# Kernel optimization log

Hardware: AMD Instinct MI355X
Metric: run time of the kernel (lower is better)

## Reference

```python
import math
import jax
import jax.numpy as jnp
import numpy as np

MUL = 32            # multiplicity of 0e and 1o in irreps_in/out
N_NODES = 50000
N_EDGES = 800000
N_BASIS = 10
N_HID = 100
NUM_NEIGHBORS = 16.0


def setup_inputs() -> dict:
    key = jax.random.key(0)
    ks = jax.random.split(key, 14)
    return {
        "node_input": jax.random.normal(ks[0], (N_NODES, 4 * MUL), jnp.float32),
        "node_attr": jnp.ones((N_NODES, 1), jnp.float32),
        "edge_src": jax.random.randint(ks[1], (N_EDGES,), 0, N_NODES, dtype=jnp.int32),
        "edge_dst": jax.random.randint(ks[2], (N_EDGES,), 0, N_NODES, dtype=jnp.int32),
        "edge_attr": jax.random.normal(ks[3], (N_EDGES, 4), jnp.float32),
        "edge_length_embedded": jax.random.uniform(ks[4], (N_EDGES, N_BASIS), dtype=jnp.float32),
        "W_sc0": jax.random.normal(ks[5], (MUL, MUL), jnp.float32),
        "W_sc1": jax.random.normal(ks[6], (MUL, MUL), jnp.float32),
        "W_l10": jax.random.normal(ks[7], (MUL, MUL), jnp.float32),
        "W_l11": jax.random.normal(ks[8], (MUL, MUL), jnp.float32),
        "W_l20": jax.random.normal(ks[9], (2 * MUL, MUL), jnp.float32),
        "W_l21": jax.random.normal(ks[10], (2 * MUL, MUL), jnp.float32),
        "W_fc1": jax.random.normal(ks[11], (N_BASIS, N_HID), jnp.float32),
        "W_fc2": jax.random.normal(ks[12], (N_HID, 4 * MUL), jnp.float32),
    }


def _fctp(x0, x1, attr, W0, W1):
    """FullyConnectedTensorProduct with a 1x0e attr: per-irrep linear * scalar attr.
    x0: [N,U], x1: [N,U,3], attr: [N,1]. Path norm alpha = 1/sqrt(fan_in)."""
    inv = 1.0 / math.sqrt(W0.shape[0])
    o0 = attr * (x0 @ W0) * inv                                    # [N,W]
    o1 = attr[:, :, None] * jnp.einsum("nud,uw->nwd", x1, W1) * inv  # [N,W,3]
    return o0, o1


def _forward(node_input, node_attr, edge_attr, edge_length_embedded,
             W_sc0, W_sc1, W_l10, W_l11, W_l20, W_l21, W_fc1, W_fc2,
             edge_src, edge_dst):
    N = node_input.shape[0]
    x0 = node_input[:, :MUL]                       # [N,32]  0e
    x1 = node_input[:, MUL:].reshape(N, MUL, 3)    # [N,32,3] 1o

    # self-connection and lin1 (both attr is scalar 0e)
    s0, s1 = _fctp(x0, x1, node_attr, W_sc0, W_sc1)
    y0, y1 = _fctp(x0, x1, node_attr, W_l10, W_l11)

    # radial MLP -> per-edge uvu weights (weight_numel = 4*MUL)
    h = jax.nn.silu(edge_length_embedded @ W_fc1 * (1.0 / math.sqrt(N_BASIS)))
    w = h @ W_fc2 * (1.0 / math.sqrt(N_HID))       # [E,128]
    w1, w2, w3, w4 = (w[:, 0*MUL:1*MUL], w[:, 1*MUL:2*MUL],
                      w[:, 2*MUL:3*MUL], w[:, 3*MUL:4*MUL])

    # gather source node features per edge
    x0s = y0[edge_src]                              # [E,32]
    x1s = y1[edge_src]                              # [E,32,3]
    ea0 = edge_attr[:, :1]                          # [E,1]   0e
    ea1 = edge_attr[:, 1:]                          # [E,3]   1o

    # segmented uvu tensor product (CG for lmax=1, component norm)
    mid0a = w1 * x0s * ea0                                         # 0e x 0e -> 0e
    mid0b = w4 * jnp.einsum("eum,em->eu", x1s, ea1) * (1.0 / math.sqrt(3.0))  # 1o x 1o -> 0e
    mid1a = (w2 * x0s)[:, :, None] * ea1[:, None, :]               # 0e x 1o -> 1o
    mid1b = w3[:, :, None] * x1s * ea0[:, None, :]                 # 1o x 0e -> 1o
    E = edge_attr.shape[0]
    edge_features = jnp.concatenate(
        [mid0a, mid0b, mid1a.reshape(E, -1), mid1b.reshape(E, -1)], axis=1)  # [E,256]

    # scatter-add to destination nodes
    agg = jax.ops.segment_sum(edge_features, edge_dst, num_segments=N)
    agg = agg * (1.0 / math.sqrt(NUM_NEIGHBORS))

    m0 = agg[:, :2 * MUL]                           # [N,64]  0e part of irreps_mid
    m1 = agg[:, 2 * MUL:].reshape(N, 2 * MUL, 3)    # [N,64,3] 1o part
    z0, z1 = _fctp(m0, m1, node_attr, W_l20, W_l21)

    # sc output_mask is all ones (every output irrep reachable)
    c_s = math.sin(math.pi / 8.0)
    c_x = math.cos(math.pi / 8.0)
    out0 = c_s * s0 + c_x * z0
    out1 = c_s * s1 + c_x * z1
    return jnp.concatenate([out0, out1.reshape(N, -1)], axis=1)   # [N,128]


def reference(node_input, node_attr, edge_src, edge_dst, edge_attr, edge_length_embedded,
              W_sc0, W_sc1, W_l10, W_l11, W_l20, W_l21, W_fc1, W_fc2):
    return _forward(node_input, node_attr, edge_attr, edge_length_embedded,
                    W_sc0, W_sc1, W_l10, W_l11, W_l20, W_l21, W_fc1, W_fc2,
                    edge_src, edge_dst)
```

## Files before the change

### kernel.cpp

```cpp
#include <hip/hip_runtime.h>
#include <hip/hip_bf16.h>

#define MUL 32
#define F4 128
#define NB 10
#define NH 100
#define EROW 136
#define FROW 72
#define XROW 136
#define REC 48

#define INV_SQRT32 0.17677669529663687f
#define INV_SQRT10 0.31622776601683794f
#define INV_SQRT100 0.1f
#define INV_SQRT3 0.5773502691896258f
#define AGG_SCALE 0.25f
#define INV8 0.125f
#define C_S 0.3826834323650898f
#define C_X 0.9238795325112867f
#define CS32 (C_S * INV_SQRT32)
#define CX8 (C_X * INV8)

typedef __attribute__((ext_vector_type(8))) short short8;
typedef __attribute__((ext_vector_type(4))) float float4v;

__device__ __forceinline__ float bf2f(__hip_bfloat16 v) { return __bfloat162float(v); }
__device__ __forceinline__ unsigned short f2b(float x) {
    __hip_bfloat16 b = __float2bfloat16(x);
    return *(unsigned short*)&b;
}
__device__ __forceinline__ float b2f(unsigned short u) {
    __hip_bfloat16 b;
    *(unsigned short*)&b = u;
    return __bfloat162float(b);
}
__device__ __forceinline__ float ldin(const void* p, size_t i, int f) {
    return f ? ((const float*)p)[i] : bf2f(((const __hip_bfloat16*)p)[i]);
}

__device__ __forceinline__ void barrier_lds() {
    asm volatile("s_waitcnt lgkmcnt(0)" ::: "memory");
    __builtin_amdgcn_s_barrier();
}

__global__ void detect_dtype_kernel(const void* __restrict__ node_attr, int* __restrict__ flag) {
    unsigned w = *(const unsigned*)node_attr;
    *flag = (w == 0x3F800000u) ? 1 : 0;
}

__global__ __launch_bounds__(256) void prep_kernel(
    const void* __restrict__ Wfc1,
    const void* __restrict__ Wfc2,
    const void* __restrict__ Wl20,
    const void* __restrict__ Wl21,
    const void* __restrict__ Wl10,
    const void* __restrict__ Wl11,
    const void* __restrict__ Wsc0,
    const void* __restrict__ Wsc1,
    const int* __restrict__ flagp,
    unsigned short* __restrict__ w1t,
    unsigned short* __restrict__ w2t,
    unsigned short* __restrict__ w20t,
    unsigned short* __restrict__ w21t,
    unsigned short* __restrict__ w10t,
    unsigned short* __restrict__ w11t,
    unsigned short* __restrict__ wsc0t,
    unsigned short* __restrict__ wsc1t)
{
    int f = *flagp;
    int gi = blockIdx.x * 256 + threadIdx.x;
    if (gi < 128 * 128) {
        int n = gi >> 7, k = gi & 127;
        w2t[gi] = (k < NH) ? f2b(ldin(Wfc2, (size_t)k * 128 + n, f)) : 0;
    }
    if (gi < 32 * 64) {
        int v = gi >> 6, u = gi & 63;
        w20t[gi] = f2b(ldin(Wl20, (size_t)u * 32 + v, f));
        w21t[gi] = f2b(ldin(Wl21, (size_t)u * 32 + v, f));
    }
    if (gi < 112 * 32) {
        int n = gi >> 5, k = gi & 31;
        w1t[gi] = (k < NB && n < NH) ? f2b(ldin(Wfc1, (size_t)k * NH + n, f)) : 0;
    }
    if (gi < 1024) {
        int c = gi >> 5, u = gi & 31;
        w10t[gi]  = f2b(ldin(Wl10, (size_t)u * 32 + c, f));
        w11t[gi]  = f2b(ldin(Wl11, (size_t)u * 32 + c, f));
        wsc0t[gi] = f2b(ldin(Wsc0, (size_t)u * 32 + c, f));
        wsc1t[gi] = f2b(ldin(Wsc1, (size_t)u * 32 + c, f));
    }
}

__global__ __launch_bounds__(256) void hist_kernel(
    const int* __restrict__ edst, int* __restrict__ cnt, int E)
{
    int i = blockIdx.x * 256 + threadIdx.x;
    if (i < E) atomicAdd(&cnt[edst[i]], 1);
}

__global__ __launch_bounds__(1024) void scanA_kernel(
    int* __restrict__ cnt, int* __restrict__ bsum, int N)
{
    __shared__ int wsum[16];
    int t = threadIdx.x, lane = t & 63, wid = t >> 6;
    int i = blockIdx.x * 1024 + t;
    int v = (i < N) ? cnt[i] : 0;
    int x = v;
#pragma unroll
    for (int d = 1; d < 64; d <<= 1) { int yv = __shfl_up(x, d); if (lane >= d) x += yv; }
    if (lane == 63) wsum[wid] = x;
    __syncthreads();
    if (wid == 0 && lane < 16) {
        int s = wsum[lane];
#pragma unroll
        for (int d = 1; d < 16; d <<= 1) { int yv = __shfl_up(s, d); if (lane >= d) s += yv; }
        wsum[lane] = s;
    }
    __syncthreads();
    int pre = (wid > 0 ? wsum[wid - 1] : 0);
    if (i < N) cnt[i] = pre + x - v;
    if (t == 0) bsum[blockIdx.x] = wsum[15];
}

__global__ __launch_bounds__(64) void scanB_kernel(int* __restrict__ bsum, int nb)
{
    int t = threadIdx.x;
    int carry = 0;
    for (int c0 = 0; c0 < nb; c0 += 64) {
        int idx = c0 + t;
        int v = (idx < nb) ? bsum[idx] : 0;
        int x = v;
#pragma unroll
        for (int d = 1; d < 64; d <<= 1) { int yv = __shfl_up(x, d); if (t >= d) x += yv; }
        if (idx < nb) bsum[idx] = carry + x - v;
        carry += __shfl(x, 63);
    }
}

__global__ __launch_bounds__(1024) void scanC_kernel(
    int* __restrict__ cnt, const int* __restrict__ bsum, int N)
{
    int i = blockIdx.x * 1024 + threadIdx.x;
    if (i < N) cnt[i] += bsum[blockIdx.x];
}

__global__ __launch_bounds__(256) void scatter_build_kernel(
    const int* __restrict__ edst,
    const int* __restrict__ esrc,
    const void* __restrict__ eattr,
    const void* __restrict__ ele,
    const int* __restrict__ flagp,
    int* __restrict__ cnt,
    unsigned char* __restrict__ rec, int E)
{
    int i = blockIdx.x * 256 + threadIdx.x;
    if (i >= E) return;
    int f = *flagp;
    int d = edst[i];
    int p = atomicAdd(&cnt[d], 1);

    unsigned e0 = f2b(ldin(ele, (size_t)i * NB + 0, f));
    unsigned e1 = f2b(ldin(ele, (size_t)i * NB + 1, f));
    unsigned e2 = f2b(ldin(ele, (size_t)i * NB + 2, f));
    unsigned e3 = f2b(ldin(ele, (size_t)i * NB + 3, f));
    unsigned e4 = f2b(ldin(ele, (size_t)i * NB + 4, f));
    unsigned e5 = f2b(ldin(ele, (size_t)i * NB + 5, f));
    unsigned e6 = f2b(ldin(ele, (size_t)i * NB + 6, f));
    unsigned e7 = f2b(ldin(ele, (size_t)i * NB + 7, f));
    unsigned e8 = f2b(ldin(ele, (size_t)i * NB + 8, f));
    unsigned e9 = f2b(ldin(ele, (size_t)i * NB + 9, f));
    float ea0 = ldin(eattr, (size_t)i * 4 + 0, f);
    float ea1 = ldin(eattr, (size_t)i * 4 + 1, f);
    float ea2 = ldin(eattr, (size_t)i * 4 + 2, f);
    float ea3 = ldin(eattr, (size_t)i * 4 + 3, f);

    unsigned char* r = rec + (size_t)p * REC;
    *(int4*)(r + 0)  = make_int4(esrc[i], d, (int)(e0 | (e1 << 16)), (int)(e2 | (e3 << 16)));
    *(int4*)(r + 16) = make_int4((int)(e4 | (e5 << 16)), (int)(e6 | (e7 << 16)), (int)(e8 | (e9 << 16)), 0);
    *(float4*)(r + 32) = make_float4(ea0, ea1, ea2, ea3);
}

__global__ __launch_bounds__(256) void node_y_kernel(
    const void* __restrict__ node_input,
    const void* __restrict__ node_attr,
    const unsigned short* __restrict__ w10t,
    const unsigned short* __restrict__ w11t,
    const int* __restrict__ flagp,
    unsigned short* __restrict__ y, int N)
{
    __shared__ __align__(16) unsigned short sXp[64 * XROW];
    __shared__ float sAt[64];
    int f = *flagp;
    int t = threadIdx.x;
    int n0 = blockIdx.x * 64;
    for (int i = t; i < 64 * 128; i += 256) {
        int n = i >> 7, c = i & 127;
        float v = (n0 + n < N) ? ldin(node_input, (size_t)(n0 + n) * F4 + c, f) : 0.f;
        int slot = (c < 32) ? c : 32 + ((c - 32) % 3) * 32 + (c - 32) / 3;
        sXp[n * XROW + slot] = f2b(v);
    }
    if (t < 64) sAt[t] = (n0 + t < N) ? ldin(node_attr, n0 + t, f) : 0.f;
    __syncthreads();

    int w = t >> 6, lane = t & 63, lm = lane & 15, quad = lane >> 4;
    int arow = (w * 16 + lm) * XROW;
    short8 ax0 = *(const short8*)(sXp + arow + quad * 8);
    short8 ax1[3];
#pragma unroll
    for (int d = 0; d < 3; d++)
        ax1[d] = *(const short8*)(sXp + arow + 32 + d * 32 + quad * 8);

#pragma unroll
    for (int seg = 0; seg < 4; seg++) {
        short8 a = (seg == 0) ? ax0 : ax1[seg - 1];
        const unsigned short* wt = (seg == 0) ? w10t : w11t;
#pragma unroll
        for (int nt = 0; nt < 2; nt++) {
            float4v c1 = (float4v){0.f, 0.f, 0.f, 0.f};
            short8 b = *(const short8*)(wt + (nt * 16 + lm) * 32 + quad * 8);
            c1 = __builtin_amdgcn_mfma_f32_16x16x32_bf16(a, b, c1, 0, 0, 0);
#pragma unroll
            for (int r = 0; r < 4; r++) {
                int nl = w * 16 + quad * 4 + r;
                int n = n0 + nl;
                if (n < N)
                    y[(size_t)n * F4 + seg * 32 + nt * 16 + lm] =
                        f2b(c1[r] * sAt[nl] * INV_SQRT32);
            }
        }
    }
}

#define SM_ELEB  0
#define SM_HW    4096
#define SM_DST   21504
#define SM_TOTAL 21760

__global__ __launch_bounds__(256, 6) void fused_edge_kernel(
    const unsigned char* __restrict__ rec,
    const unsigned short* __restrict__ y,
    const unsigned short* __restrict__ w1t,
    const unsigned short* __restrict__ w2t,
    const unsigned short* __restrict__ w20t,
    const unsigned short* __restrict__ w21t,
    float* __restrict__ agg,
    int E)
{
    __shared__ __align__(16) char smem[SM_TOTAL];
    unsigned short* sEleB = (unsigned short*)(smem + SM_ELEB);
    unsigned short* sHW = (unsigned short*)(smem + SM_HW);
    int* sDst = (int*)(smem + SM_DST);

    int t = threadIdx.x;
    int base = blockIdx.x * 64;
    int ne = E - base;
    if (ne > 64) ne = 64;

    int w = t >> 6, lane = t & 63;
    int lm = lane & 15, quad = lane >> 4;
    int em = w * 16 + lm;

    int src = (em < ne) ? *(const int*)(rec + (size_t)(base + em) * REC) : 0;
    float4 ea4 = (em < ne) ? *(const float4*)(rec + (size_t)(base + em) * REC + 32)
                           : make_float4(0.f, 0.f, 0.f, 0.f);
    const unsigned short* yrg = y + (size_t)src * 128;
    short8 x0  = *(const short8*)(yrg + quad * 8);
    short8 xd0 = *(const short8*)(yrg + 32 + quad * 8);
    short8 xd1 = *(const short8*)(yrg + 64 + quad * 8);
    short8 xd2 = *(const short8*)(yrg + 96 + quad * 8);
    short8 w1f[7];
#pragma unroll
    for (int nt = 0; nt < 7; nt++)
        w1f[nt] = *(const short8*)(w1t + (nt * 16 + lm) * 32 + quad * 8);

    if (t < 64)
        sDst[t] = (t < ne) ? *(const int*)(rec + (size_t)(base + t) * REC + 4) : -1;
    for (int i = t; i < 64 * 32; i += 256) {
        int e = i >> 5, k = i & 31;
        unsigned short v = 0;
        if (k < NB && e < ne)
            v = *(const unsigned short*)(rec + (size_t)(base + e) * REC + 8 + 2 * k);
        sEleB[i] = v;
    }
    barrier_lds();

    {
        short8 a = *(const short8*)(sEleB + (w * 16 + lm) * 32 + quad * 8);
#pragma unroll
        for (int nt = 0; nt < 7; nt++) {
            float4v c1 = (float4v){0.f, 0.f, 0.f, 0.f};
            c1 = __builtin_amdgcn_mfma_f32_16x16x32_bf16(a, w1f[nt], c1, 0, 0, 0);
            int ch = nt * 16 + lm;
#pragma unroll
            for (int r = 0; r < 4; r++) {
                int row = w * 16 + quad * 4 + r;
                float hv = 0.f;
                if (ch < NH) {
                    float aa = c1[r] * INV_SQRT10;
                    hv = aa / (1.f + __expf(-aa));
                }
                sHW[row * EROW + ch] = f2b(hv);
            }
        }
        int e = t >> 2, seg = t & 3;
        *(uint2*)(sHW + e * EROW + 112 + seg * 4) = (uint2){0u, 0u};
    }
    barrier_lds();

    short8 hfr[4];
#pragma unroll
    for (int kc = 0; kc < 4; kc++)
        hfr[kc] = *(const short8*)(sHW + (w * 16 + lm) * EROW + kc * 32 + quad * 8);
    barrier_lds();
#pragma unroll
    for (int nt = 0; nt < 8; nt++) {
        float4v c2 = (float4v){0.f, 0.f, 0.f, 0.f};
#pragma unroll
        for (int kc = 0; kc < 4; kc++) {
            short8 b = *(const short8*)(w2t + (nt * 16 + lm) * 128 + kc * 32 + quad * 8);
            c2 = __builtin_amdgcn_mfma_f32_16x16x32_bf16(hfr[kc], b, c2, 0, 0, 0);
        }
#pragma unroll
        for (int r = 0; r < 4; r++)
            sHW[(w * 16 + quad * 4 + r) * EROW + nt * 16 + lm] = f2b(c2[r] * INV_SQRT100);
    }
    barrier_lds();

    {
        const unsigned short* wr = sHW + em * EROW;
        short8 wA = *(const short8*)(wr + quad * 8);
        short8 wB = *(const short8*)(wr + 32 + quad * 8);
        short8 wC = *(const short8*)(wr + 64 + quad * 8);
        short8 wD = *(const short8*)(wr + 96 + quad * 8);
        float ea0 = ea4.x;
        float e1x = ea4.y;
        float e1y = ea4.z;
        float e1z = ea4.w;
        float ea0S = ea0 * AGG_SCALE;
        float s3 = AGG_SCALE * INV_SQRT3;

        short8 f00, f01, f10, f11, f20, f21, f30, f31;
#pragma unroll
        for (int j = 0; j < 8; j++) {
            float x0f = b2f((unsigned short)x0[j]);
            float d0f = b2f((unsigned short)xd0[j]);
            float d1f = b2f((unsigned short)xd1[j]);
            float d2f = b2f((unsigned short)xd2[j]);
            f00[j] = (short)f2b(b2f((unsigned short)wA[j]) * x0f * ea0S);
            float tt = d0f * e1x + d1f * e1y + d2f * e1z;
            f01[j] = (short)f2b(b2f((unsigned short)wD[j]) * tt * s3);
            float p = b2f((unsigned short)wB[j]) * x0f * AGG_SCALE;
            f10[j] = (short)f2b(p * e1x);
            f20[j] = (short)f2b(p * e1y);
            f30[j] = (short)f2b(p * e1z);
            float q = b2f((unsigned short)wC[j]) * ea0S;
            f11[j] = (short)f2b(q * d0f);
            f21[j] = (short)f2b(q * d1f);
            f31[j] = (short)f2b(q * d2f);
        }

        barrier_lds();
        unsigned short* sFeatT = (unsigned short*)smem;
#pragma unroll
        for (int g = 0; g < 4; g++) {
            const unsigned short* wt = g ? w21t : w20t;
            short8 ak0 = (g == 0) ? f00 : (g == 1) ? f10 : (g == 2) ? f20 : f30;
            short8 ak1 = (g == 0) ? f01 : (g == 1) ? f11 : (g == 2) ? f21 : f31;
#pragma unroll
            for (int nt = 0; nt < 2; nt++) {
                float4v acc = (float4v){0.f, 0.f, 0.f, 0.f};
                short8 b0 = *(const short8*)(wt + (nt * 16 + lm) * 64 + quad * 8);
                short8 b1 = *(const short8*)(wt + (nt * 16 + lm) * 64 + 32 + quad * 8);
                acc = __builtin_amdgcn_mfma_f32_16x16x32_bf16(ak0, b0, acc, 0, 0, 0);
                acc = __builtin_amdgcn_mfma_f32_16x16x32_bf16(ak1, b1, acc, 0, 0, 0);
                int ch = (g == 0) ? (nt * 16 + lm) : (32 + (g - 1) * 32 + nt * 16 + lm);
                short4 sv;
                sv.x = (short)f2b(acc[0]);
                sv.y = (short)f2b(acc[1]);
                sv.z = (short)f2b(acc[2]);
                sv.w = (short)f2b(acc[3]);
                *(short4*)(sFeatT + ch * FROW + (w * 16 + quad * 4)) = sv;
            }
        }
        barrier_lds();

        if (t < 128) {
            int c = t;
            unsigned long long m =
                __ballot((lane == 0) ? 1 : (sDst[lane] != sDst[lane - 1]));
            const unsigned short* fr = sFeatT + c * FROW;
            short8 fv[8];
#pragma unroll
            for (int q8 = 0; q8 < 8; q8++)
                fv[q8] = *(const short8*)(fr + q8 * 8);
            float s = 0.f;
            int rs = 0;
#pragma unroll
            for (int e = 0; e < 64; e++) {
                s += b2f((unsigned short)fv[e >> 3][e & 7]);
                bool fl = (e == 63) || ((m >> (e + 1)) & 1ull);
                if (fl) {
                    int d = sDst[e];
                    if (d >= 0) {
                        if (rs > 0 && e < ne - 1) agg[(size_t)d * F4 + c] = s;
                        else atomicAdd(&agg[(size_t)d * F4 + c], s);
                    }
                    s = 0.f;
                    rs = e + 1;
                }
            }
        }
    }
}

__global__ __launch_bounds__(256) void out_kernel(
    const void* __restrict__ node_input,
    const void* __restrict__ node_attr,
    const unsigned short* __restrict__ wsc0t,
    const unsigned short* __restrict__ wsc1t,
    const float* __restrict__ agg,
    const int* __restrict__ flagp,
    void* __restrict__ out, int N)
{
    __shared__ __align__(16) unsigned short sXp[64 * XROW];
    __shared__ float sAt[64];
    int f = *flagp;
    int t = threadIdx.x;
    int n0 = blockIdx.x * 64;
    for (int i = t; i < 64 * 128; i += 256) {
        int n = i >> 7, c = i & 127;
        float v = (n0 + n < N) ? ldin(node_input, (size_t)(n0 + n) * F4 + c, f) : 0.f;
        int slot = (c < 32) ? c : 32 + ((c - 32) % 3) * 32 + (c - 32) / 3;
        sXp[n * XROW + slot] = f2b(v);
    }
    if (t < 64) sAt[t] = (n0 + t < N) ? ldin(node_attr, n0 + t, f) : 0.f;
    __syncthreads();

    int w = t >> 6, lane = t & 63, lm = lane & 15, quad = lane >> 4;
    int arow = (w * 16 + lm) * XROW;
    short8 ax0 = *(const short8*)(sXp + arow + quad * 8);
    short8 ax1[3];
#pragma unroll
    for (int d = 0; d < 3; d++)
        ax1[d] = *(const short8*)(sXp + arow + 32 + d * 32 + quad * 8);

#pragma unroll
    for (int seg = 0; seg < 4; seg++) {
        short8 a = (seg == 0) ? ax0 : ax1[seg - 1];
        const unsigned short* wt = (seg == 0) ? wsc0t : wsc1t;
#pragma unroll
        for (int nt = 0; nt < 2; nt++) {
            float4v c1 = (float4v){0.f, 0.f, 0.f, 0.f};
            short8 b = *(const short8*)(wt + (nt * 16 + lm) * 32 + quad * 8);
            c1 = __builtin_amdgcn_mfma_f32_16x16x32_bf16(a, b, c1, 0, 0, 0);
            int col = nt * 16 + lm;
#pragma unroll
            for (int r = 0; r < 4; r++) {
                int nl = w * 16 + quad * 4 + r;
                int n = n0 + nl;
                if (n < N) {
                    float z = agg[(size_t)n * F4 + seg * 32 + col];
                    float val = sAt[nl] * (CS32 * c1[r] + CX8 * z);
                    int c = (seg == 0) ? col : 32 + col * 3 + (seg - 1);
                    size_t oi = (size_t)n * F4 + c;
                    if (f) ((float*)out)[oi] = val;
                    else   ((__hip_bfloat16*)out)[oi] = __float2bfloat16(val);
                }
            }
        }
    }
}

extern "C" void kernel_launch(void* const* d_in, const int* in_sizes, int n_in,
                              void* d_out, int out_size, void* d_ws, size_t ws_size,
                              hipStream_t stream) {
    const void* node_input = d_in[0];
    const void* node_attr  = d_in[1];
    const int* edge_src    = (const int*)d_in[2];
    const int* edge_dst    = (const int*)d_in[3];
    const void* edge_attr  = d_in[4];
    const void* ele        = d_in[5];
    const void* Wsc0       = d_in[6];
    const void* Wsc1       = d_in[7];
    const void* Wl10       = d_in[8];
    const void* Wl11       = d_in[9];
    const void* Wl20       = d_in[10];
    const void* Wl21       = d_in[11];
    const void* Wfc1       = d_in[12];
    const void* Wfc2       = d_in[13];

    int N = in_sizes[0] / F4;
    int E = in_sizes[2];

    char* ws = (char*)d_ws;
    int* flag = (int*)ws;
    unsigned short* y = (unsigned short*)(ws + 64);
    size_t y_b = (size_t)N * F4 * 2;
    float* agg = (float*)(ws + 64 + y_b);
    size_t agg_b = (size_t)N * F4 * 4;
    size_t off = 64 + y_b + agg_b;
    unsigned short* w2t  = (unsigned short*)(ws + off);
    unsigned short* w20t = (unsigned short*)(ws + off + 32768);
    unsigned short* w21t = (unsigned short*)(ws + off + 36864);
    unsigned short* w1t  = (unsigned short*)(ws + off + 40960);
    size_t off2 = off + 49152;
    unsigned short* w10t  = (unsigned short*)(ws + off2);
    unsigned short* w11t  = (unsigned short*)(ws + off2 + 2048);
    unsigned short* wsc0t = (unsigned short*)(ws + off2 + 4096);
    unsigned short* wsc1t = (unsigned short*)(ws + off2 + 6144);
    size_t off3 = off2 + 8192;
    int* cnt = (int*)(ws + off3);
    size_t cnt_b = ((size_t)N * 4 + 63) & ~(size_t)63;
    int* bsum = (int*)(ws + off3 + cnt_b);
    size_t bsum_b = 4096;
    unsigned char* rec = (unsigned char*)(ws + off3 + cnt_b + bsum_b);

    int nscan = (N + 1023) / 1024;

    detect_dtype_kernel<<<1, 1, 0, stream>>>(node_attr, flag);
    prep_kernel<<<64, 256, 0, stream>>>(Wfc1, Wfc2, Wl20, Wl21, Wl10, Wl11, Wsc0, Wsc1,
                                        flag, w1t, w2t, w20t, w21t,
                                        w10t, w11t, wsc0t, wsc1t);
    (void)hipMemsetAsync(cnt, 0, (size_t)N * 4, stream);
    (void)hipMemsetAsync(agg, 0, agg_b, stream);

    hist_kernel<<<(E + 255) / 256, 256, 0, stream>>>(edge_dst, cnt, E);
    scanA_kernel<<<nscan, 1024, 0, stream>>>(cnt, bsum, N);
    scanB_kernel<<<1, 64, 0, stream>>>(bsum, nscan);
    scanC_kernel<<<nscan, 1024, 0, stream>>>(cnt, bsum, N);
    scatter_build_kernel<<<(E + 255) / 256, 256, 0, stream>>>(
        edge_dst, edge_src, edge_attr, ele, flag, cnt, rec, E);

    node_y_kernel<<<(N + 63) / 64, 256, 0, stream>>>(node_input, node_attr,
                                                     w10t, w11t, flag, y, N);

    fused_edge_kernel<<<(E + 63) / 64, 256, 0, stream>>>(
        rec, y, w1t, w2t, w20t, w21t, agg, E);

    out_kernel<<<(N + 63) / 64, 256, 0, stream>>>(node_input, node_attr,
                                                  wsc0t, wsc1t, agg, flag, d_out, N);
}
```

Before: 579.4 us.

## Merge setup kernels, fuse node-y with histogram, process two edge tiles per block

Replaces the dtype-detect kernel and two memsets with a single init kernel, and merges node_y and the edge histogram into one launch split by block index. Scan steps B and C are folded together, with each block summing its preceding block totals itself. The fused edge kernel now handles two 64-edge tiles per block, issuing both tiles' gathers up front so the second tile's loads overlap the first tile's compute. The point is to cut launch overhead and hide gather latency, at the cost of more registers per thread and an extra barrier per tile.

```diff
diff --git a/kernel.cpp b/kernel.cpp
--- a/kernel.cpp
+++ b/kernel.cpp
@@ -43,9 +43,20 @@
     __builtin_amdgcn_s_barrier();
 }
 
-__global__ void detect_dtype_kernel(const void* __restrict__ node_attr, int* __restrict__ flag) {
-    unsigned w = *(const unsigned*)node_attr;
-    *flag = (w == 0x3F800000u) ? 1 : 0;
+__global__ __launch_bounds__(256) void init_kernel(
+    const void* __restrict__ node_attr, int* __restrict__ flag,
+    int* __restrict__ cnt, float* __restrict__ agg, int N)
+{
+    int gi = blockIdx.x * 256 + threadIdx.x;
+    if (gi == 0) {
+        unsigned w = *(const unsigned*)node_attr;
+        *flag = (w == 0x3F800000u) ? 1 : 0;
+    }
+    for (int i = gi; i < N; i += gridDim.x * 256) cnt[i] = 0;
+    float4* a4 = (float4*)agg;
+    int n4 = N * 32;
+    for (int i = gi; i < n4; i += gridDim.x * 256)
+        a4[i] = make_float4(0.f, 0.f, 0.f, 0.f);
 }
 
 __global__ __launch_bounds__(256) void prep_kernel(
@@ -91,11 +102,63 @@
     }
 }
 
-__global__ __launch_bounds__(256) void hist_kernel(
-    const int* __restrict__ edst, int* __restrict__ cnt, int E)
-{
-    int i = blockIdx.x * 256 + threadIdx.x;
-    if (i < E) atomicAdd(&cnt[edst[i]], 1);
+__global__ __launch_bounds__(256) void nodeY_hist_kernel(
+    const void* __restrict__ node_input,
+    const void* __restrict__ node_attr,
+    const unsigned short* __restrict__ w10t,
+    const unsigned short* __restrict__ w11t,
+    const int* __restrict__ flagp,
+    unsigned short* __restrict__ y, int N,
+    const int* __restrict__ edst, int* __restrict__ cnt, int E, int nyb)
+{
+    __shared__ __align__(16) unsigned short sXp[64 * XROW];
+    __shared__ float sAt[64];
+    int t = threadIdx.x;
+
+    if (blockIdx.x >= nyb) {
+        int i = (blockIdx.x - nyb) * 256 + t;
+        if (i < E) atomicAdd(&cnt[edst[i]], 1);
+        return;
+    }
+
+    int f = *flagp;
+    int n0 = blockIdx.x * 64;
+    for (int i = t; i < 64 * 128; i += 256) {
+        int n = i >> 7, c = i & 127;
+        float v = (n0 + n < N) ? ldin(node_input, (size_t)(n0 + n) * F4 + c, f) : 0.f;
+        int slot = (c < 32) ? c : 32 + ((c - 32) % 3) * 32 + (c - 32) / 3;
+        sXp[n * XROW + slot] = f2b(v);
+    }
+    if (t < 64) sAt[t] = (n0 + t < N) ? ldin(node_attr, n0 + t, f) : 0.f;
+    __syncthreads();
+
+    int w = t >> 6, lane = t & 63, lm = lane & 15, quad = lane >> 4;
+    int arow = (w * 16 + lm) * XROW;
+    short8 ax0 = *(const short8*)(sXp + arow + quad * 8);
+    short8 ax1[3];
+#pragma unroll
+    for (int d = 0; d < 3; d++)
+        ax1[d] = *(const short8*)(sXp + arow + 32 + d * 32 + quad * 8);
+
+#pragma unroll
+    for (int seg = 0; seg < 4; seg++) {
+        short8 a = (seg == 0) ? ax0 : ax1[seg - 1];
+        const unsigned short* wt = (seg == 0) ? w10t : w11t;
+#pragma unroll
+        for (int nt = 0; nt < 2; nt++) {
+            float4v c1 = (float4v){0.f, 0.f, 0.f, 0.f};
+            short8 b = *(const short8*)(wt + (nt * 16 + lm) * 32 + quad * 8);
+            c1 = __builtin_amdgcn_mfma_f32_16x16x32_bf16(a, b, c1, 0, 0, 0);
+#pragma unroll
+            for (int r = 0; r < 4; r++) {
+                int nl = w * 16 + quad * 4 + r;
+                int n = n0 + nl;
+                if (n < N)
+                    y[(size_t)n * F4 + seg * 32 + nt * 16 + lm] =
+                        f2b(c1[r] * sAt[nl] * INV_SQRT32);
+            }
+        }
+    }
 }
 
 __global__ __launch_bounds__(1024) void scanA_kernel(
@@ -122,26 +185,21 @@
     if (t == 0) bsum[blockIdx.x] = wsum[15];
 }
 
-__global__ __launch_bounds__(64) void scanB_kernel(int* __restrict__ bsum, int nb)
-{
+__global__ __launch_bounds__(1024) void scanC2_kernel(
+    int* __restrict__ cnt, const int* __restrict__ bsum, int N, int nb)
+{
+    __shared__ int soff;
     int t = threadIdx.x;
-    int carry = 0;
-    for (int c0 = 0; c0 < nb; c0 += 64) {
-        int idx = c0 + t;
-        int v = (idx < nb) ? bsum[idx] : 0;
-        int x = v;
-#pragma unroll
-        for (int d = 1; d < 64; d <<= 1) { int yv = __shfl_up(x, d); if (t >= d) x += yv; }
-        if (idx < nb) bsum[idx] = carry + x - v;
-        carry += __shfl(x, 63);
-    }
-}
-
-__global__ __launch_bounds__(1024) void scanC_kernel(
-    int* __restrict__ cnt, const int* __restrict__ bsum, int N)
-{
-    int i = blockIdx.x * 1024 + threadIdx.x;
-    if (i < N) cnt[i] += bsum[blockIdx.x];
+    if (t < 64) {
+        int p = 0;
+        for (int j = t; j < (int)blockIdx.x; j += 64) p += bsum[j];
+#pragma unroll
+        for (int d = 1; d < 64; d <<= 1) p += __shfl_xor(p, d);
+        if (t == 0) soff = p;
+    }
+    __syncthreads();
+    int i = blockIdx.x * 1024 + t;
+    if (i < N) cnt[i] += soff;
 }
 
 __global__ __launch_bounds__(256) void scatter_build_kernel(
@@ -180,57 +238,6 @@
     *(float4*)(r + 32) = make_float4(ea0, ea1, ea2, ea3);
 }
 
-__global__ __launch_bounds__(256) void node_y_kernel(
-    const void* __restrict__ node_input,
-    const void* __restrict__ node_attr,
-    const unsigned short* __restrict__ w10t,
-    const unsigned short* __restrict__ w11t,
-    const int* __restrict__ flagp,
-    unsigned short* __restrict__ y, int N)
-{
-    __shared__ __align__(16) unsigned short sXp[64 * XROW];
-    __shared__ float sAt[64];
-    int f = *flagp;
-    int t = threadIdx.x;
-    int n0 = blockIdx.x * 64;
-    for (int i = t; i < 64 * 128; i += 256) {
-        int n = i >> 7, c = i & 127;
-        float v = (n0 + n < N) ? ldin(node_input, (size_t)(n0 + n) * F4 + c, f) : 0.f;
-        int slot = (c < 32) ? c : 32 + ((c - 32) % 3) * 32 + (c - 32) / 3;
-        sXp[n * XROW + slot] = f2b(v);
-    }
-    if (t < 64) sAt[t] = (n0 + t < N) ? ldin(node_attr, n0 + t, f) : 0.f;
-    __syncthreads();
-
-    int w = t >> 6, lane = t & 63, lm = lane & 15, quad = lane >> 4;
-    int arow = (w * 16 + lm) * XROW;
-    short8 ax0 = *(const short8*)(sXp + arow + quad * 8);
-    short8 ax1[3];
-#pragma unroll
-    for (int d = 0; d < 3; d++)
-        ax1[d] = *(const short8*)(sXp + arow + 32 + d * 32 + quad * 8);
-
-#pragma unroll
-    for (int seg = 0; seg < 4; seg++) {
-        short8 a = (seg == 0) ? ax0 : ax1[seg - 1];
-        const unsigned short* wt = (seg == 0) ? w10t : w11t;
-#pragma unroll
-        for (int nt = 0; nt < 2; nt++) {
-            float4v c1 = (float4v){0.f, 0.f, 0.f, 0.f};
-            short8 b = *(const short8*)(wt + (nt * 16 + lm) * 32 + quad * 8);
-            c1 = __builtin_amdgcn_mfma_f32_16x16x32_bf16(a, b, c1, 0, 0, 0);
-#pragma unroll
-            for (int r = 0; r < 4; r++) {
-                int nl = w * 16 + quad * 4 + r;
-                int n = n0 + nl;
-                if (n < N)
-                    y[(size_t)n * F4 + seg * 32 + nt * 16 + lm] =
-                        f2b(c1[r] * sAt[nl] * INV_SQRT32);
-            }
-        }
-    }
-}
-
 #define SM_ELEB  0
 #define SM_HW    4096
 #define SM_DST   21504
@@ -252,91 +259,94 @@
     int* sDst = (int*)(smem + SM_DST);
 
     int t = threadIdx.x;
-    int base = blockIdx.x * 64;
-    int ne = E - base;
-    if (ne > 64) ne = 64;
+    int base0 = blockIdx.x * 128;
+    int neA = E - base0;        if (neA > 64) neA = 64;  if (neA < 0) neA = 0;
+    int neB = E - base0 - 64;   if (neB > 64) neB = 64;  if (neB < 0) neB = 0;
 
     int w = t >> 6, lane = t & 63;
     int lm = lane & 15, quad = lane >> 4;
     int em = w * 16 + lm;
 
-    int src = (em < ne) ? *(const int*)(rec + (size_t)(base + em) * REC) : 0;
-    float4 ea4 = (em < ne) ? *(const float4*)(rec + (size_t)(base + em) * REC + 32)
-                           : make_float4(0.f, 0.f, 0.f, 0.f);
-    const unsigned short* yrg = y + (size_t)src * 128;
-    short8 x0  = *(const short8*)(yrg + quad * 8);
-    short8 xd0 = *(const short8*)(yrg + 32 + quad * 8);
-    short8 xd1 = *(const short8*)(yrg + 64 + quad * 8);
-    short8 xd2 = *(const short8*)(yrg + 96 + quad * 8);
-    short8 w1f[7];
-#pragma unroll
-    for (int nt = 0; nt < 7; nt++)
-        w1f[nt] = *(const short8*)(w1t + (nt * 16 + lm) * 32 + quad * 8);
-
-    if (t < 64)
-        sDst[t] = (t < ne) ? *(const int*)(rec + (size_t)(base + t) * REC + 4) : -1;
-    for (int i = t; i < 64 * 32; i += 256) {
-        int e = i >> 5, k = i & 31;
-        unsigned short v = 0;
-        if (k < NB && e < ne)
-            v = *(const unsigned short*)(rec + (size_t)(base + e) * REC + 8 + 2 * k);
-        sEleB[i] = v;
-    }
-    barrier_lds();
-
-    {
-        short8 a = *(const short8*)(sEleB + (w * 16 + lm) * 32 + quad * 8);
-#pragma unroll
-        for (int nt = 0; nt < 7; nt++) {
-            float4v c1 = (float4v){0.f, 0.f, 0.f, 0.f};
-            c1 = __builtin_amdgcn_mfma_f32_16x16x32_bf16(a, w1f[nt], c1, 0, 0, 0);
-            int ch = nt * 16 + lm;
-#pragma unroll
-            for (int r = 0; r < 4; r++) {
-                int row = w * 16 + quad * 4 + r;
-                float hv = 0.f;
-                if (ch < NH) {
-                    float aa = c1[r] * INV_SQRT10;
-                    hv = aa / (1.f + __expf(-aa));
+    int srcA = (em < neA) ? *(const int*)(rec + (size_t)(base0 + em) * REC) : 0;
+    float4 eaA = (em < neA) ? *(const float4*)(rec + (size_t)(base0 + em) * REC + 32)
+                            : make_float4(0.f, 0.f, 0.f, 0.f);
+    int srcB = (em < neB) ? *(const int*)(rec + (size_t)(base0 + 64 + em) * REC) : 0;
+    float4 eaB = (em < neB) ? *(const float4*)(rec + (size_t)(base0 + 64 + em) * REC + 32)
+                            : make_float4(0.f, 0.f, 0.f, 0.f);
+    const unsigned short* yrgA = y + (size_t)srcA * 128;
+    short8 xA0  = *(const short8*)(yrgA + quad * 8);
+    short8 xAd0 = *(const short8*)(yrgA + 32 + quad * 8);
+    short8 xAd1 = *(const short8*)(yrgA + 64 + quad * 8);
+    short8 xAd2 = *(const short8*)(yrgA + 96 + quad * 8);
+    const unsigned short* yrgB = y + (size_t)srcB * 128;
+    short8 xB0  = *(const short8*)(yrgB + quad * 8);
+    short8 xBd0 = *(const short8*)(yrgB + 32 + quad * 8);
+    short8 xBd1 = *(const short8*)(yrgB + 64 + quad * 8);
+    short8 xBd2 = *(const short8*)(yrgB + 96 + quad * 8);
+
+    auto process_tile = [&](int baseT, int neT, short8 x0, short8 xd0,
+                            short8 xd1, short8 xd2, float4 ea4) {
+        if (t < 64)
+            sDst[t] = (t < neT) ? *(const int*)(rec + (size_t)(baseT + t) * REC + 4) : -1;
+        for (int i = t; i < 64 * 32; i += 256) {
+            int e = i >> 5, k = i & 31;
+            unsigned short v = 0;
+            if (k < NB && e < neT)
+                v = *(const unsigned short*)(rec + (size_t)(baseT + e) * REC + 8 + 2 * k);
+            sEleB[i] = v;
+        }
+        barrier_lds();
+
+        {
+            short8 a = *(const short8*)(sEleB + (w * 16 + lm) * 32 + quad * 8);
+#pragma unroll
+            for (int nt = 0; nt < 7; nt++) {
+                float4v c1 = (float4v){0.f, 0.f, 0.f, 0.f};
+                short8 b = *(const short8*)(w1t + (nt * 16 + lm) * 32 + quad * 8);
+                c1 = __builtin_amdgcn_mfma_f32_16x16x32_bf16(a, b, c1, 0, 0, 0);
+                int ch = nt * 16 + lm;
+#pragma unroll
+                for (int r = 0; r < 4; r++) {
+                    int row = w * 16 + quad * 4 + r;
+                    float hv = 0.f;
+                    if (ch < NH) {
+                        float aa = c1[r] * INV_SQRT10;
+                        hv = aa / (1.f + __expf(-aa));
+                    }
+                    sHW[row * EROW + ch] = f2b(hv);
                 }
-                sHW[row * EROW + ch] = f2b(hv);
             }
-        }
-        int e = t >> 2, seg = t & 3;
-        *(uint2*)(sHW + e * EROW + 112 + seg * 4) = (uint2){0u, 0u};
-    }
-    barrier_lds();
-
-    short8 hfr[4];
-#pragma unroll
-    for (int kc = 0; kc < 4; kc++)
-        hfr[kc] = *(const short8*)(sHW + (w * 16 + lm) * EROW + kc * 32 + quad * 8);
-    barrier_lds();
-#pragma unroll
-    for (int nt = 0; nt < 8; nt++) {
-        float4v c2 = (float4v){0.f, 0.f, 0.f, 0.f};
-#pragma unroll
-        for (int kc = 0; kc < 4; kc++) {
-            short8 b = *(const short8*)(w2t + (nt * 16 + lm) * 128 + kc * 32 + quad * 8);
-            c2 = __builtin_amdgcn_mfma_f32_16x16x32_bf16(hfr[kc], b, c2, 0, 0, 0);
-        }
-#pragma unroll
-        for (int r = 0; r < 4; r++)
-            sHW[(w * 16 + quad * 4 + r) * EROW + nt * 16 + lm] = f2b(c2[r] * INV_SQRT100);
-    }
-    barrier_lds();
-
-    {
+            int e = t >> 2, seg = t & 3;
+            *(uint2*)(sHW + e * EROW + 112 + seg * 4) = (uint2){0u, 0u};
+        }
+        barrier_lds();
+
+        short8 hfr[4];
+#pragma unroll
+        for (int kc = 0; kc < 4; kc++)
+            hfr[kc] = *(const short8*)(sHW + (w * 16 + lm) * EROW + kc * 32 + quad * 8);
+        barrier_lds();
+#pragma unroll
+        for (int nt = 0; nt < 8; nt++) {
+            float4v c2 = (float4v){0.f, 0.f, 0.f, 0.f};
+#pragma unroll
+            for (int kc = 0; kc < 4; kc++) {
+                short8 b = *(const short8*)(w2t + (nt * 16 + lm) * 128 + kc * 32 + quad * 8);
+                c2 = __builtin_amdgcn_mfma_f32_16x16x32_bf16(hfr[kc], b, c2, 0, 0, 0);
+            }
+#pragma unroll
+            for (int r = 0; r < 4; r++)
+                sHW[(w * 16 + quad * 4 + r) * EROW + nt * 16 + lm] = f2b(c2[r] * INV_SQRT100);
+        }
+        barrier_lds();
+
         const unsigned short* wr = sHW + em * EROW;
         short8 wA = *(const short8*)(wr + quad * 8);
         short8 wB = *(const short8*)(wr + 32 + quad * 8);
         short8 wC = *(const short8*)(wr + 64 + quad * 8);
         short8 wD = *(const short8*)(wr + 96 + quad * 8);
-        float ea0 = ea4.x;
-        float e1x = ea4.y;
-        float e1y = ea4.z;
-        float e1z = ea4.w;
-        float ea0S = ea0 * AGG_SCALE;
+        float ea0S = ea4.x * AGG_SCALE;
+        float e1x = ea4.y, e1y = ea4.z, e1z = ea4.w;
         float s3 = AGG_SCALE * INV_SQRT3;
 
         short8 f00, f01, f10, f11, f20, f21, f30, f31;
@@ -384,15 +394,18 @@
         }
         barrier_lds();
 
+        unsigned long long m = 0;
+        short8 fv[8];
+        if (t < 128) {
+            m = __ballot((lane == 0) ? 1 : (sDst[lane] != sDst[lane - 1]));
+            const unsigned short* fr = sFeatT + t * FROW;
+#pragma unroll
+            for (int q8 = 0; q8 < 8; q8++)
+                fv[q8] = *(const short8*)(fr + q8 * 8);
+        }
+        barrier_lds();
         if (t < 128) {
             int c = t;
-            unsigned long long m =
-                __ballot((lane == 0) ? 1 : (sDst[lane] != sDst[lane - 1]));
-            const unsigned short* fr = sFeatT + c * FROW;
-            short8 fv[8];
-#pragma unroll
-            for (int q8 = 0; q8 < 8; q8++)
-                fv[q8] = *(const short8*)(fr + q8 * 8);
             float s = 0.f;
             int rs = 0;
 #pragma unroll
@@ -402,7 +415,7 @@
                 if (fl) {
                     int d = sDst[e];
                     if (d >= 0) {
-                        if (rs > 0 && e < ne - 1) agg[(size_t)d * F4 + c] = s;
+                        if (rs > 0 && e < neT - 1) agg[(size_t)d * F4 + c] = s;
                         else atomicAdd(&agg[(size_t)d * F4 + c], s);
                     }
                     s = 0.f;
@@ -410,7 +423,11 @@
                 }
             }
         }
-    }
+        barrier_lds();
+    };
+
+    if (neA > 0) process_tile(base0, neA, xA0, xAd0, xAd1, xAd2, eaA);
+    if (neB > 0) process_tile(base0 + 64, neB, xB0, xBd0, xBd1, xBd2, eaB);
 }
 
 __global__ __launch_bounds__(256) void out_kernel(
@@ -516,25 +533,22 @@
     unsigned char* rec = (unsigned char*)(ws + off3 + cnt_b + bsum_b);
 
     int nscan = (N + 1023) / 1024;
-
-    detect_dtype_kernel<<<1, 1, 0, stream>>>(node_attr, flag);
+    int nyb = (N + 63) / 64;
+
+    init_kernel<<<2048, 256, 0, stream>>>(node_attr, flag, cnt, agg, N);
     prep_kernel<<<64, 256, 0, stream>>>(Wfc1, Wfc2, Wl20, Wl21, Wl10, Wl11, Wsc0, Wsc1,
                                         flag, w1t, w2t, w20t, w21t,
                                         w10t, w11t, wsc0t, wsc1t);
-    (void)hipMemsetAsync(cnt, 0, (size_t)N * 4, stream);
-    (void)hipMemsetAsync(agg, 0, agg_b, stream);
-
-    hist_kernel<<<(E + 255) / 256, 256, 0, stream>>>(edge_dst, cnt, E);
+
+    nodeY_hist_kernel<<<nyb + (E + 255) / 256, 256, 0, stream>>>(
+        node_input, node_attr, w10t, w11t, flag, y, N, edge_dst, cnt, E, nyb);
+
     scanA_kernel<<<nscan, 1024, 0, stream>>>(cnt, bsum, N);
-    scanB_kernel<<<1, 64, 0, stream>>>(bsum, nscan);
-    scanC_kernel<<<nscan, 1024, 0, stream>>>(cnt, bsum, N);
+    scanC2_kernel<<<nscan, 1024, 0, stream>>>(cnt, bsum, N, nscan);
     scatter_build_kernel<<<(E + 255) / 256, 256, 0, stream>>>(
         edge_dst, edge_src, edge_attr, ele, flag, cnt, rec, E);
 
-    node_y_kernel<<<(N + 63) / 64, 256, 0, stream>>>(node_input, node_attr,
-                                                     w10t, w11t, flag, y, N);
-
-    fused_edge_kernel<<<(E + 63) / 64, 256, 0, stream>>>(
+    fused_edge_kernel<<<(E + 127) / 128, 256, 0, stream>>>(
         rec, y, w1t, w2t, w20t, w21t, agg, E);
 
     out_kernel<<<(N + 63) / 64, 256, 0, stream>>>(node_input, node_attr,
```

Measured after the change: 589.4 us. Within noise of the previous version (+1.7%).
